# Kernel optimization log

Hardware: AMD Instinct MI355X
Metric: run time of the kernel (lower is better)

The kernel has to match this reference:

```python
import jax, jax.numpy as jnp
import numpy as np

NUM_TOKENS = 8192
MODEL_DIM = 4096
NUM_EXPERTS = 64
CAPACITY_FACTOR = 1.0


def setup_inputs() -> dict:
    key = jax.random.key(0)
    k1, k2 = jax.random.split(key)
    inp = jax.random.normal(k1, (NUM_TOKENS, MODEL_DIM), dtype=jnp.float32)
    wg = jax.random.normal(k2, (NUM_EXPERTS, MODEL_DIM), dtype=jnp.float32) * (1.0 / np.sqrt(MODEL_DIM))
    return {"input": inp, "wg_weight": wg}


def reference(input, wg_weight):
    # logits = input @ wg.T  -> [T, E]
    logits = jnp.einsum('td,ed->te', input, wg_weight)
    num_tokens, num_experts = logits.shape
    capacity = int(CAPACITY_FACTOR * ((num_tokens + num_experts - 1) // num_experts))

    indices1_s = jnp.argmax(logits, axis=1)                      # [T]
    mask1 = jax.nn.one_hot(indices1_s, num_experts, dtype=logits.dtype)  # [T, E]
    gates = jax.nn.softmax(logits, axis=1)                       # [T, E]
    gates1_s = jnp.sum(gates * mask1, axis=1)                    # [T]

    # locations: position of each token within its chosen expert's queue
    # (exclusive cumsum over the one-hot mask, gathered at the chosen expert)
    locations1 = jnp.cumsum(mask1, axis=0) - 1.0                 # [T, E]
    locations1_s = jnp.sum(locations1 * mask1, axis=1).astype(jnp.int32)  # [T]

    # load-balancing aux loss (float32 branch of the original)
    me = jnp.sum(gates, axis=0)                                  # [E]
    ce = jnp.sum(mask1, axis=0)                                  # [E]
    l_aux = jnp.sum(me * ce) * (num_experts / (num_tokens * num_tokens))

    return (l_aux, indices1_s.astype(jnp.int32), locations1_s, gates1_s)
```

## Files before the change

### kernel.cpp

```cpp
#include <hip/hip_runtime.h>

namespace {
constexpr int TOK = 8192;
constexpr int DIM = 4096;
constexpr int NE  = 64;
constexpr int TB  = 128;
constexpr int KS  = 8;
constexpr int KR  = DIM / KS;
constexpr int BK  = 32;
constexpr int NT  = TOK / TB;
constexpr int NITER = KR / BK;
constexpr int ATS = TB + 4;
constexpr int BTS = NE + 4;
constexpr int GB  = 64;
constexpr int NCH = TOK / GB;
}

__global__ __launch_bounds__(128) void gemm_split(
    const float* __restrict__ A, const float* __restrict__ W,
    float* __restrict__ partial) {
  __shared__ float As[BK * ATS];
  __shared__ float Bs[BK * BTS];
  const int bid  = blockIdx.x;
  const int tile = bid & (NT - 1);
  const int ks   = bid / NT;
  const int t0   = tile * TB;
  const int k0   = ks * KR;
  const int tid  = threadIdx.x;

  float4 ra[8];
  float4 rb[4];

  {
    const int kb = k0;
#pragma unroll
    for (int j = 0; j < 8; ++j) {
      const int idx = tid + 128 * j;
      const int rr = idx >> 3, cc = (idx & 7) * 4;
      ra[j] = *(const float4*)(A + (size_t)(t0 + rr) * DIM + kb + cc);
    }
#pragma unroll
    for (int j = 0; j < 4; ++j) {
      const int idx = tid + 128 * j;
      const int ee = idx >> 3, cc = (idx & 7) * 4;
      rb[j] = *(const float4*)(W + (size_t)ee * DIM + kb + cc);
    }
  }

  float acc[8][8];
#pragma unroll
  for (int i = 0; i < 8; ++i)
#pragma unroll
    for (int j = 0; j < 8; ++j) acc[i][j] = 0.0f;

  const int ta = (tid >> 3) * 8;
  const int ea = (tid & 7) * 8;

  for (int it = 0; it < NITER; ++it) {
    __syncthreads();
#pragma unroll
    for (int j = 0; j < 8; ++j) {
      const int idx = tid + 128 * j;
      const int rr = idx >> 3, cc = (idx & 7) * 4;
      As[(cc + 0) * ATS + rr] = ra[j].x;
      As[(cc + 1) * ATS + rr] = ra[j].y;
      As[(cc + 2) * ATS + rr] = ra[j].z;
      As[(cc + 3) * ATS + rr] = ra[j].w;
    }
#pragma unroll
    for (int j = 0; j < 4; ++j) {
      const int idx = tid + 128 * j;
      const int ee = idx >> 3, cc = (idx & 7) * 4;
      Bs[(cc + 0) * BTS + ee] = rb[j].x;
      Bs[(cc + 1) * BTS + ee] = rb[j].y;
      Bs[(cc + 2) * BTS + ee] = rb[j].z;
      Bs[(cc + 3) * BTS + ee] = rb[j].w;
    }
    __syncthreads();
    if (it + 1 < NITER) {
      const int kb = k0 + (it + 1) * BK;
#pragma unroll
      for (int j = 0; j < 8; ++j) {
        const int idx = tid + 128 * j;
        const int rr = idx >> 3, cc = (idx & 7) * 4;
        ra[j] = *(const float4*)(A + (size_t)(t0 + rr) * DIM + kb + cc);
      }
#pragma unroll
      for (int j = 0; j < 4; ++j) {
        const int idx = tid + 128 * j;
        const int ee = idx >> 3, cc = (idx & 7) * 4;
        rb[j] = *(const float4*)(W + (size_t)ee * DIM + kb + cc);
      }
    }
#pragma unroll 8
    for (int k = 0; k < BK; ++k) {
      const float4 a0 = *(const float4*)(As + k * ATS + ta);
      const float4 a1 = *(const float4*)(As + k * ATS + ta + 4);
      const float4 b0 = *(const float4*)(Bs + k * BTS + ea);
      const float4 b1 = *(const float4*)(Bs + k * BTS + ea + 4);
      const float av[8] = {a0.x, a0.y, a0.z, a0.w, a1.x, a1.y, a1.z, a1.w};
      const float bv[8] = {b0.x, b0.y, b0.z, b0.w, b1.x, b1.y, b1.z, b1.w};
#pragma unroll
      for (int i = 0; i < 8; ++i)
#pragma unroll
        for (int j = 0; j < 8; ++j) acc[i][j] += av[i] * bv[j];
    }
  }

  float* P = partial + (size_t)ks * TOK * NE;
#pragma unroll
  for (int i = 0; i < 8; ++i) {
    const int t = t0 + ta + i;
    *(float4*)(P + (size_t)t * NE + ea) =
        make_float4(acc[i][0], acc[i][1], acc[i][2], acc[i][3]);
    *(float4*)(P + (size_t)t * NE + ea + 4) =
        make_float4(acc[i][4], acc[i][5], acc[i][6], acc[i][7]);
  }
}

__global__ __launch_bounds__(256) void gating(
    const float* __restrict__ partial, float* __restrict__ out,
    int* __restrict__ idx_int, int* __restrict__ rankp,
    int* __restrict__ hist, float* __restrict__ me) {
  __shared__ float L[GB * 65];
  __shared__ float mx[GB];
  __shared__ float dninv[GB];
  __shared__ int   eid[GB];
  const int b = blockIdx.x, tid = threadIdx.x;
  const size_t base = (size_t)b * GB * NE;

#pragma unroll
  for (int j = 0; j < (GB * NE) / 256; ++j) {
    const int idx = tid + 256 * j;
    float s = 0.0f;
#pragma unroll
    for (int k = 0; k < KS; ++k)
      s += partial[(size_t)k * TOK * NE + base + idx];
    L[(idx >> 6) * 65 + (idx & 63)] = s;
  }
  __syncthreads();

  if (tid < GB) {
    const int t = tid;
    float m = -3.0e38f; int bi = 0;
    for (int e = 0; e < NE; ++e) {
      const float v = L[t * 65 + e];
      if (v > m) { m = v; bi = e; }
    }
    float s = 0.0f;
    for (int e = 0; e < NE; ++e) s += __expf(L[t * 65 + e] - m);
    const float inv = 1.0f / s;
    mx[t] = m; dninv[t] = inv; eid[t] = bi;
    const int gt = b * GB + t;
    out[1 + gt]           = (float)bi;
    out[1 + 2 * TOK + gt] = inv;
    idx_int[gt] = bi;
  }
  __syncthreads();

  if (tid < GB) {
    const int t = tid, e = eid[t];
    int r = 0;
    for (int j = 0; j < t; ++j) r += (eid[j] == e) ? 1 : 0;
    rankp[b * GB + t] = r;
    int c = 0;
    for (int t2 = 0; t2 < GB; ++t2) c += (eid[t2] == tid) ? 1 : 0;
    hist[b * NE + tid] = c;
  } else if (tid < 2 * GB) {
    const int e = tid - GB;
    float s = 0.0f;
    for (int t2 = 0; t2 < GB; ++t2)
      s += __expf(L[t2 * 65 + e] - mx[t2]) * dninv[t2];
    atomicAdd(&me[e], s);
  }
}

__global__ __launch_bounds__(256) void finalize(
    const int* __restrict__ idx_int, const int* __restrict__ rankp,
    const int* __restrict__ hist, const float* __restrict__ me,
    float* __restrict__ out) {
  __shared__ int   H[NCH * NE];
  __shared__ float CE[NE];
  const int tid = threadIdx.x;
  for (int j = tid; j < NCH * NE; j += 256) H[j] = hist[j];
  __syncthreads();
  if (tid < NE) {
    int run = 0;
    for (int b = 0; b < NCH; ++b) {
      const int v = H[b * NE + tid];
      H[b * NE + tid] = run;
      run += v;
    }
    CE[tid] = (float)run;
  }
  __syncthreads();
  if (tid < 64) {
    float p = me[tid] * CE[tid];
#pragma unroll
    for (int off = 32; off > 0; off >>= 1) p += __shfl_down(p, off);
    if (tid == 0) out[0] = p * ((float)NE / ((float)TOK * (float)TOK));
  }
  for (int i = tid; i < TOK; i += 256) {
    const int e = idx_int[i];
    out[1 + TOK + i] = (float)(H[(i >> 6) * NE + e] + rankp[i]);
  }
}

extern "C" void kernel_launch(void* const* d_in, const int* in_sizes, int n_in,
                              void* d_out, int out_size, void* d_ws, size_t ws_size,
                              hipStream_t stream) {
  const float* A = (const float*)d_in[0];
  const float* W = (const float*)d_in[1];
  float* out = (float*)d_out;
  char* ws = (char*)d_ws;

  float* partial = (float*)ws;
  const size_t poff = (size_t)KS * TOK * NE * sizeof(float);
  float* me     = (float*)(ws + poff);
  int*  idx_int = (int*)(ws + poff + 1024);
  int*  rankp   = idx_int + TOK;
  int*  hist    = rankp + TOK;

  hipMemsetAsync(me, 0, NE * sizeof(float), stream);
  hipLaunchKernelGGL(gemm_split, dim3(NT * KS), dim3(128), 0, stream, A, W, partial);
  hipLaunchKernelGGL(gating, dim3(NCH), dim3(256), 0, stream, partial, out,
                     idx_int, rankp, hist, me);
  hipLaunchKernelGGL(finalize, dim3(1), dim3(256), 0, stream, idx_int, rankp,
                     hist, me, out);
}
```

Measured before the change: 226.5 us.

## Use split-fp16 MFMA for router GEMM and drop atomic aux-loss reduction

The FP32 SIMT outer-product GEMM is replaced with MFMA 16x16x32 f16 instructions. Each fp32 operand is split into hi and lo halves, and three MFMAs per tile approximate fp32 accuracy. The block size grows to 256 threads with four wavefronts. The gating kernel now writes per-chunk expert sums instead of using atomics, which also removes the memset, and finalize parallelizes its prefix scan across four segments. The risk is small precision differences that could flip argmax on near ties.

After: 212.0 us. 1.07x faster.

```diff
diff --git a/kernel.cpp b/kernel.cpp
--- a/kernel.cpp
+++ b/kernel.cpp
@@ -10,118 +10,143 @@
 constexpr int BK  = 32;
 constexpr int NT  = TOK / TB;
 constexpr int NITER = KR / BK;
-constexpr int ATS = TB + 4;
-constexpr int BTS = NE + 4;
+constexpr int LSTR = 40;
 constexpr int GB  = 64;
 constexpr int NCH = TOK / GB;
 }
 
-__global__ __launch_bounds__(128) void gemm_split(
+typedef _Float16 f16x8 __attribute__((ext_vector_type(8)));
+typedef _Float16 f16x4 __attribute__((ext_vector_type(4)));
+typedef float    f32x4 __attribute__((ext_vector_type(4)));
+
+__global__ __launch_bounds__(256) void gemm_split(
     const float* __restrict__ A, const float* __restrict__ W,
     float* __restrict__ partial) {
-  __shared__ float As[BK * ATS];
-  __shared__ float Bs[BK * BTS];
+  __shared__ _Float16 sm[(2 * TB + 2 * NE) * LSTR];
+  _Float16* sAhi = sm;
+  _Float16* sAlo = sm + TB * LSTR;
+  _Float16* sWhi = sm + 2 * TB * LSTR;
+  _Float16* sWlo = sm + 2 * TB * LSTR + NE * LSTR;
+
   const int bid  = blockIdx.x;
   const int tile = bid & (NT - 1);
   const int ks   = bid / NT;
   const int t0   = tile * TB;
   const int k0   = ks * KR;
   const int tid  = threadIdx.x;
-
-  float4 ra[8];
-  float4 rb[4];
-
-  {
-    const int kb = k0;
-#pragma unroll
-    for (int j = 0; j < 8; ++j) {
-      const int idx = tid + 128 * j;
-      const int rr = idx >> 3, cc = (idx & 7) * 4;
-      ra[j] = *(const float4*)(A + (size_t)(t0 + rr) * DIM + kb + cc);
-    }
+  const int w    = tid >> 6;
+  const int lane = tid & 63;
+  const int col  = lane & 15;
+  const int quad = lane >> 4;
+
+  float4 ra[4], rw[2];
+  {
 #pragma unroll
     for (int j = 0; j < 4; ++j) {
-      const int idx = tid + 128 * j;
-      const int ee = idx >> 3, cc = (idx & 7) * 4;
-      rb[j] = *(const float4*)(W + (size_t)ee * DIM + kb + cc);
-    }
-  }
-
-  float acc[8][8];
-#pragma unroll
-  for (int i = 0; i < 8; ++i)
-#pragma unroll
-    for (int j = 0; j < 8; ++j) acc[i][j] = 0.0f;
-
-  const int ta = (tid >> 3) * 8;
-  const int ea = (tid & 7) * 8;
+      const int f4 = tid + 256 * j;
+      const int tk = f4 >> 3, kc = (f4 & 7) * 4;
+      ra[j] = *(const float4*)(A + (size_t)(t0 + tk) * DIM + k0 + kc);
+    }
+#pragma unroll
+    for (int j = 0; j < 2; ++j) {
+      const int f4 = tid + 256 * j;
+      const int ee = f4 >> 3, kc = (f4 & 7) * 4;
+      rw[j] = *(const float4*)(W + (size_t)ee * DIM + k0 + kc);
+    }
+  }
+
+  f32x4 acc[2][4];
+#pragma unroll
+  for (int i = 0; i < 2; ++i)
+#pragma unroll
+    for (int j = 0; j < 4; ++j) acc[i][j] = (f32x4)0.0f;
 
   for (int it = 0; it < NITER; ++it) {
     __syncthreads();
 #pragma unroll
-    for (int j = 0; j < 8; ++j) {
-      const int idx = tid + 128 * j;
-      const int rr = idx >> 3, cc = (idx & 7) * 4;
-      As[(cc + 0) * ATS + rr] = ra[j].x;
-      As[(cc + 1) * ATS + rr] = ra[j].y;
-      As[(cc + 2) * ATS + rr] = ra[j].z;
-      As[(cc + 3) * ATS + rr] = ra[j].w;
-    }
-#pragma unroll
     for (int j = 0; j < 4; ++j) {
-      const int idx = tid + 128 * j;
-      const int ee = idx >> 3, cc = (idx & 7) * 4;
-      Bs[(cc + 0) * BTS + ee] = rb[j].x;
-      Bs[(cc + 1) * BTS + ee] = rb[j].y;
-      Bs[(cc + 2) * BTS + ee] = rb[j].z;
-      Bs[(cc + 3) * BTS + ee] = rb[j].w;
+      const int f4 = tid + 256 * j;
+      const int tk = f4 >> 3, kc = (f4 & 7) * 4;
+      const float4 r = ra[j];
+      const _Float16 hx = (_Float16)r.x, hy = (_Float16)r.y,
+                     hz = (_Float16)r.z, hw = (_Float16)r.w;
+      *(f16x4*)(sAhi + tk * LSTR + kc) = (f16x4){hx, hy, hz, hw};
+      *(f16x4*)(sAlo + tk * LSTR + kc) =
+          (f16x4){(_Float16)(r.x - (float)hx), (_Float16)(r.y - (float)hy),
+                  (_Float16)(r.z - (float)hz), (_Float16)(r.w - (float)hw)};
+    }
+#pragma unroll
+    for (int j = 0; j < 2; ++j) {
+      const int f4 = tid + 256 * j;
+      const int ee = f4 >> 3, kc = (f4 & 7) * 4;
+      const float4 r = rw[j];
+      const _Float16 hx = (_Float16)r.x, hy = (_Float16)r.y,
+                     hz = (_Float16)r.z, hw = (_Float16)r.w;
+      *(f16x4*)(sWhi + ee * LSTR + kc) = (f16x4){hx, hy, hz, hw};
+      *(f16x4*)(sWlo + ee * LSTR + kc) =
+          (f16x4){(_Float16)(r.x - (float)hx), (_Float16)(r.y - (float)hy),
+                  (_Float16)(r.z - (float)hz), (_Float16)(r.w - (float)hw)};
     }
     __syncthreads();
     if (it + 1 < NITER) {
       const int kb = k0 + (it + 1) * BK;
 #pragma unroll
-      for (int j = 0; j < 8; ++j) {
-        const int idx = tid + 128 * j;
-        const int rr = idx >> 3, cc = (idx & 7) * 4;
-        ra[j] = *(const float4*)(A + (size_t)(t0 + rr) * DIM + kb + cc);
-      }
-#pragma unroll
       for (int j = 0; j < 4; ++j) {
-        const int idx = tid + 128 * j;
-        const int ee = idx >> 3, cc = (idx & 7) * 4;
-        rb[j] = *(const float4*)(W + (size_t)ee * DIM + kb + cc);
-      }
-    }
-#pragma unroll 8
-    for (int k = 0; k < BK; ++k) {
-      const float4 a0 = *(const float4*)(As + k * ATS + ta);
-      const float4 a1 = *(const float4*)(As + k * ATS + ta + 4);
-      const float4 b0 = *(const float4*)(Bs + k * BTS + ea);
-      const float4 b1 = *(const float4*)(Bs + k * BTS + ea + 4);
-      const float av[8] = {a0.x, a0.y, a0.z, a0.w, a1.x, a1.y, a1.z, a1.w};
-      const float bv[8] = {b0.x, b0.y, b0.z, b0.w, b1.x, b1.y, b1.z, b1.w};
-#pragma unroll
-      for (int i = 0; i < 8; ++i)
-#pragma unroll
-        for (int j = 0; j < 8; ++j) acc[i][j] += av[i] * bv[j];
-    }
+        const int f4 = tid + 256 * j;
+        const int tk = f4 >> 3, kc = (f4 & 7) * 4;
+        ra[j] = *(const float4*)(A + (size_t)(t0 + tk) * DIM + kb + kc);
+      }
+#pragma unroll
+      for (int j = 0; j < 2; ++j) {
+        const int f4 = tid + 256 * j;
+        const int ee = f4 >> 3, kc = (f4 & 7) * 4;
+        rw[j] = *(const float4*)(W + (size_t)ee * DIM + kb + kc);
+      }
+    }
+    f16x8 ah[2], al[2], bh[4], bl[4];
+#pragma unroll
+    for (int mt = 0; mt < 2; ++mt) {
+      const int r = w * 32 + mt * 16 + col;
+      ah[mt] = *(const f16x8*)(sAhi + r * LSTR + quad * 8);
+      al[mt] = *(const f16x8*)(sAlo + r * LSTR + quad * 8);
+    }
+#pragma unroll
+    for (int et = 0; et < 4; ++et) {
+      const int e = et * 16 + col;
+      bh[et] = *(const f16x8*)(sWhi + e * LSTR + quad * 8);
+      bl[et] = *(const f16x8*)(sWlo + e * LSTR + quad * 8);
+    }
+#pragma unroll
+    for (int mt = 0; mt < 2; ++mt)
+#pragma unroll
+      for (int et = 0; et < 4; ++et) {
+        acc[mt][et] = __builtin_amdgcn_mfma_f32_16x16x32_f16(
+            ah[mt], bh[et], acc[mt][et], 0, 0, 0);
+        acc[mt][et] = __builtin_amdgcn_mfma_f32_16x16x32_f16(
+            ah[mt], bl[et], acc[mt][et], 0, 0, 0);
+        acc[mt][et] = __builtin_amdgcn_mfma_f32_16x16x32_f16(
+            al[mt], bh[et], acc[mt][et], 0, 0, 0);
+      }
   }
 
   float* P = partial + (size_t)ks * TOK * NE;
 #pragma unroll
-  for (int i = 0; i < 8; ++i) {
-    const int t = t0 + ta + i;
-    *(float4*)(P + (size_t)t * NE + ea) =
-        make_float4(acc[i][0], acc[i][1], acc[i][2], acc[i][3]);
-    *(float4*)(P + (size_t)t * NE + ea + 4) =
-        make_float4(acc[i][4], acc[i][5], acc[i][6], acc[i][7]);
-  }
+  for (int mt = 0; mt < 2; ++mt)
+#pragma unroll
+    for (int et = 0; et < 4; ++et) {
+      const int e = et * 16 + col;
+#pragma unroll
+      for (int r = 0; r < 4; ++r) {
+        const int t = t0 + w * 32 + mt * 16 + quad * 4 + r;
+        P[(size_t)t * NE + e] = acc[mt][et][r];
+      }
+    }
 }
 
 __global__ __launch_bounds__(256) void gating(
     const float* __restrict__ partial, float* __restrict__ out,
     int* __restrict__ idx_int, int* __restrict__ rankp,
-    int* __restrict__ hist, float* __restrict__ me) {
+    int* __restrict__ hist, float* __restrict__ me_part) {
   __shared__ float L[GB * 65];
   __shared__ float mx[GB];
   __shared__ float dninv[GB];
@@ -171,38 +196,64 @@
     float s = 0.0f;
     for (int t2 = 0; t2 < GB; ++t2)
       s += __expf(L[t2 * 65 + e] - mx[t2]) * dninv[t2];
-    atomicAdd(&me[e], s);
+    me_part[b * NE + e] = s;
   }
 }
 
 __global__ __launch_bounds__(256) void finalize(
     const int* __restrict__ idx_int, const int* __restrict__ rankp,
-    const int* __restrict__ hist, const float* __restrict__ me,
+    const int* __restrict__ hist, const float* __restrict__ me_part,
     float* __restrict__ out) {
   __shared__ int   H[NCH * NE];
+  __shared__ int   SEG[4 * NE];
+  __shared__ float MEp[4 * NE];
   __shared__ float CE[NE];
   const int tid = threadIdx.x;
+  const int e = tid & 63, seg = tid >> 6;
+
   for (int j = tid; j < NCH * NE; j += 256) H[j] = hist[j];
+  {
+    float s = 0.0f;
+    for (int c = seg * 32; c < seg * 32 + 32; ++c) s += me_part[c * NE + e];
+    MEp[seg * NE + e] = s;
+  }
+  __syncthreads();
+  {
+    int hs = 0;
+    for (int c = seg * 32; c < seg * 32 + 32; ++c) hs += H[c * NE + e];
+    SEG[seg * NE + e] = hs;
+  }
   __syncthreads();
   if (tid < NE) {
     int run = 0;
-    for (int b = 0; b < NCH; ++b) {
-      const int v = H[b * NE + tid];
-      H[b * NE + tid] = run;
+    for (int s2 = 0; s2 < 4; ++s2) {
+      const int v = SEG[s2 * NE + tid];
+      SEG[s2 * NE + tid] = run;
       run += v;
     }
     CE[tid] = (float)run;
   }
   __syncthreads();
+  {
+    int run = SEG[seg * NE + e];
+    for (int c = seg * 32; c < seg * 32 + 32; ++c) {
+      const int v = H[c * NE + e];
+      H[c * NE + e] = run;
+      run += v;
+    }
+  }
   if (tid < 64) {
-    float p = me[tid] * CE[tid];
+    float p = (MEp[tid] + MEp[NE + tid] + MEp[2 * NE + tid] + MEp[3 * NE + tid])
+              * CE[tid];
 #pragma unroll
     for (int off = 32; off > 0; off >>= 1) p += __shfl_down(p, off);
     if (tid == 0) out[0] = p * ((float)NE / ((float)TOK * (float)TOK));
   }
+  __syncthreads();
+#pragma unroll 4
   for (int i = tid; i < TOK; i += 256) {
-    const int e = idx_int[i];
-    out[1 + TOK + i] = (float)(H[(i >> 6) * NE + e] + rankp[i]);
+    const int ex = idx_int[i];
+    out[1 + TOK + i] = (float)(H[(i >> 6) * NE + ex] + rankp[i]);
   }
 }
 
@@ -216,15 +267,14 @@
 
   float* partial = (float*)ws;
   const size_t poff = (size_t)KS * TOK * NE * sizeof(float);
-  float* me     = (float*)(ws + poff);
-  int*  idx_int = (int*)(ws + poff + 1024);
+  float* me_part = (float*)(ws + poff);
+  int*  idx_int = (int*)(ws + poff + NCH * NE * sizeof(float));
   int*  rankp   = idx_int + TOK;
   int*  hist    = rankp + TOK;
 
-  hipMemsetAsync(me, 0, NE * sizeof(float), stream);
-  hipLaunchKernelGGL(gemm_split, dim3(NT * KS), dim3(128), 0, stream, A, W, partial);
+  hipLaunchKernelGGL(gemm_split, dim3(NT * KS), dim3(256), 0, stream, A, W, partial);
   hipLaunchKernelGGL(gating, dim3(NCH), dim3(256), 0, stream, partial, out,
-                     idx_int, rankp, hist, me);
+                     idx_int, rankp, hist, me_part);
   hipLaunchKernelGGL(finalize, dim3(1), dim3(256), 0, stream, idx_int, rankp,
-                     hist, me, out);
-}
+                     hist, me_part, out);
+}
```
